# Kernel optimization log

Hardware: AMD Instinct MI355X
Metric: run time of the kernel (lower is better)

The kernel has to match this reference:

```python
import jax, jax.numpy as jnp
import numpy as np

ROT_DIM = 32  # rotary sub-dimension hardcoded in the original module


def apply_rope(x, rope):
    # x: [B, T, H, hd], rope: [T, ROT_DIM//2, 2]
    T = x.shape[1]
    rc = rope[:T][:, None]            # [T, 1, 16, 2]
    cos, sin = rc[..., 0], rc[..., 1]  # [T, 1, 16]
    x_rot, x_pass = x[..., :ROT_DIM], x[..., ROT_DIM:]
    x1, x2 = x_rot[..., :ROT_DIM // 2], x_rot[..., ROT_DIM // 2:]
    return jnp.concatenate([x1 * cos - x2 * sin, x2 * cos + x1 * sin, x_pass], axis=-1)


def setup_inputs() -> dict:
    key = jax.random.key(0)
    ks = jax.random.split(key, 6)
    B, T, C, H = 4, 1024, 2048, 32
    hd = C // H
    x = jax.random.normal(ks[0], (B, T, C), dtype=jnp.float32)
    mask = jnp.tril(jnp.ones((T, T), dtype=bool))  # causal, True = attend
    index = jnp.arange(T, dtype=jnp.int64) if jax.config.jax_enable_x64 else jnp.arange(T, dtype=jnp.int32)
    # realistic rotary cos/sin cache
    inv_freq = 1.0 / (10000.0 ** (np.arange(0, ROT_DIM, 2, dtype=np.float32) / ROT_DIM))
    ang = np.arange(T, dtype=np.float32)[:, None] * inv_freq[None, :]  # [T, 16]
    rope = jnp.asarray(np.stack([np.cos(ang), np.sin(ang)], axis=-1))   # [T, 16, 2]
    s = 1.0 / np.sqrt(C)
    Wqkv_w = jax.random.normal(ks[1], (3 * C, C), dtype=jnp.float32) * s
    Wqkv_b = jax.random.normal(ks[2], (3 * C,), dtype=jnp.float32) * 0.01
    out_w = jax.random.normal(ks[3], (C, C), dtype=jnp.float32) * s
    out_b = jax.random.normal(ks[4], (C,), dtype=jnp.float32) * 0.01
    k_cache = jnp.zeros((B, H, T, hd), dtype=jnp.float32)
    v_cache = jnp.zeros((B, H, T, hd), dtype=jnp.float32)
    return {"x": x, "mask": mask, "index": index, "rope": rope,
            "Wqkv_w": Wqkv_w, "Wqkv_b": Wqkv_b, "out_w": out_w, "out_b": out_b,
            "k_cache": k_cache, "v_cache": v_cache}


def reference(x, mask, index, rope, Wqkv_w, Wqkv_b, out_w, out_b, k_cache, v_cache):
    B, T, C = x.shape
    H = 32
    hd = C // H
    qkv = x @ Wqkv_w.T + Wqkv_b                 # [B, T, 3C]
    q, k, v = jnp.split(qkv, 3, axis=-1)
    q = q.reshape(B, T, H, hd)
    k = k.reshape(B, T, H, hd)
    v = v.reshape(B, T, H, hd)
    q = apply_rope(q, rope)
    k = apply_rope(k, rope)
    q = q.transpose(0, 2, 1, 3)                 # [B, H, T, hd]
    k = k.transpose(0, 2, 1, 3)
    v = v.transpose(0, 2, 1, 3)
    # KV-cache scatter update; index = arange(T) covers the full cache, so the
    # subsequent slice [:, :, :index[-1]+1] is the whole cache (static shape).
    k_full = k_cache.at[:, :, index].set(k)
    v_full = v_cache.at[:, :, index].set(v)
    scores = jnp.einsum('bhqd,bhkd->bhqk', q, k_full) / jnp.sqrt(jnp.asarray(hd, x.dtype))
    scores = jnp.where(mask, scores, jnp.finfo(x.dtype).min)
    attn = jax.nn.softmax(scores, axis=-1)
    ctx = jnp.einsum('bhqk,bhkd->bhqd', attn, v_full)
    ctx = ctx.transpose(0, 2, 1, 3).reshape(B, T, C)
    return ctx @ out_w.T + out_b
```

## Files before the change

kernel.cpp:

```cpp
#include <hip/hip_runtime.h>

typedef unsigned short u16;
typedef unsigned int u32;
typedef __bf16 bf16x8 __attribute__((ext_vector_type(8)));
typedef float floatx4 __attribute__((ext_vector_type(4)));
typedef u16 u16x4 __attribute__((ext_vector_type(4)));
typedef u16 u16x8 __attribute__((ext_vector_type(8)));
typedef u32 u32x2 __attribute__((ext_vector_type(2)));

#define B_ 4
#define T_ 1024
#define C_ 2048
#define H_ 32
#define HD_ 64

__device__ __forceinline__ float b2f(u16 u) {
    u32 x = ((u32)u) << 16;
    return __builtin_bit_cast(float, x);
}
__device__ __forceinline__ u16 f2b(float f) {
    u32 i = __builtin_bit_cast(u32, f);
    u32 r = (i + 0x7FFFu + ((i >> 16) & 1u)) >> 16;
    return (u16)r;
}
__device__ __forceinline__ u32 pack2(float a, float b) {
    const u32 ua = __builtin_bit_cast(u32, a) + 0x8000u;
    const u32 ub = __builtin_bit_cast(u32, b) + 0x8000u;
    return __builtin_amdgcn_perm(ub, ua, 0x07060302u);
}

#define GLOAD16(gp, lp) __builtin_amdgcn_global_load_lds( \
    (const __attribute__((address_space(1))) void*)(gp),  \
    (__attribute__((address_space(3))) void*)(lp), 16, 0, 0)

#define LGKM0() asm volatile("s_waitcnt lgkmcnt(0)" ::: "memory")

__global__ __launch_bounds__(256) void convert_all(const float* __restrict__ x,
                                                   const float* __restrict__ wqkv,
                                                   const float* __restrict__ outw,
                                                   u16* __restrict__ dst) {
    const int stride = gridDim.x * 256;
    for (int i = blockIdx.x * 256 + threadIdx.x; i < 6291456; i += stride) {
        const float* s;
        int off;
        if (i < 2097152) { s = x; off = i; }
        else if (i < 5242880) { s = wqkv; off = i - 2097152; }
        else { s = outw; off = i - 5242880; }
        const floatx4 v = *(const floatx4*)(s + (size_t)off * 4);
        const u32x2 h = {pack2(v.x, v.y), pack2(v.z, v.w)};
        *(u32x2*)(dst + (size_t)i * 4) = h;
    }
}

template <int MODE>
__global__ __launch_bounds__(256) void gemm_bt(const u16* __restrict__ A,
                                               const u16* __restrict__ W,
                                               const float* __restrict__ bias,
                                               const float* __restrict__ rope,
                                               void* __restrict__ o0v,
                                               u16* __restrict__ o1,
                                               u16* __restrict__ o2) {
    const int Kdim = 2048;
    __shared__ __align__(16) u16 As[128 * 64];
    __shared__ __align__(16) u16 Bs[128 * 64];

    const int tid = threadIdx.x;
    const int w = tid >> 6, lane = tid & 63;
    const int wr = w >> 1, wc = w & 1;
    const int quad = lane >> 4, l15 = lane & 15;
    const int mBase = blockIdx.y * 128, nBase = blockIdx.x * 128;

    floatx4 acc[4][4] = {};

    const int lrow = lane >> 3;
    const int lcol = ((lane & 7) ^ lrow) * 8;
    const u16* Ap = A + (size_t)(mBase + lrow) * Kdim + lcol;
    const u16* Wp = W + (size_t)(nBase + lrow) * Kdim + lcol;

    const int xk = l15 & 7;

    for (int k0 = 0; k0 < Kdim; k0 += 64) {
#pragma unroll
        for (int i = 0; i < 4; i++) {
            const int c = i * 4 + w;
            GLOAD16(Ap + (size_t)c * 8 * Kdim + k0, &As[c * 512]);
            GLOAD16(Wp + (size_t)c * 8 * Kdim + k0, &Bs[c * 512]);
        }
        __syncthreads();
#pragma unroll
        for (int ks = 0; ks < 64; ks += 32) {
            bf16x8 af[4], bfr[4];
#pragma unroll
            for (int i = 0; i < 4; i++) {
                const int co = (((ks >> 3) + quad) ^ xk) * 8;
                af[i] = *(const bf16x8*)&As[(wr * 64 + i * 16 + l15) * 64 + co];
            }
#pragma unroll
            for (int j = 0; j < 4; j++) {
                const int co = (((ks >> 3) + quad) ^ xk) * 8;
                bfr[j] = *(const bf16x8*)&Bs[(wc * 64 + j * 16 + l15) * 64 + co];
            }
#pragma unroll
            for (int i = 0; i < 4; i++)
#pragma unroll
                for (int j = 0; j < 4; j++)
                    acc[i][j] = __builtin_amdgcn_mfma_f32_16x16x32_bf16(af[i], bfr[j], acc[i][j], 0, 0, 0);
        }
        __syncthreads();
    }

    const int nq = nBase + wc * 64;
    float bv[4];
#pragma unroll
    for (int j = 0; j < 4; j++) bv[j] = bias[nq + j * 16 + l15];

    if (MODE == 0) {
        const int region = nq >> 11;
        const int h = (nq & 2047) >> 6;
        const int d = l15;
        u16* dst = (region == 0) ? (u16*)o0v : ((region == 1) ? o1 : o2);
#pragma unroll
        for (int i = 0; i < 4; i++) {
#pragma unroll
            for (int r = 0; r < 4; r++) {
                const int m = mBase + wr * 64 + i * 16 + quad * 4 + r;
                const int b = m >> 10, t = m & 1023;
                float v0 = acc[i][0][r] + bv[0];
                float v1 = acc[i][1][r] + bv[1];
                float v2 = acc[i][2][r] + bv[2];
                float v3 = acc[i][3][r] + bv[3];
                const size_t base = ((size_t)(b * H_ + h) * T_ + t) * HD_;
                if (region < 2) {
                    const float cz = rope[t * 32 + d * 2];
                    const float sz = rope[t * 32 + d * 2 + 1];
                    const float n0 = v0 * cz - v1 * sz;
                    const float n1 = v1 * cz + v0 * sz;
                    dst[base + d] = f2b(n0);
                    dst[base + 16 + d] = f2b(n1);
                } else {
                    dst[base + d] = f2b(v0);
                    dst[base + 16 + d] = f2b(v1);
                }
                dst[base + 32 + d] = f2b(v2);
                dst[base + 48 + d] = f2b(v3);
            }
        }
    } else {
        float* outf = (float*)o0v;
#pragma unroll
        for (int i = 0; i < 4; i++)
#pragma unroll
            for (int r = 0; r < 4; r++) {
                const int m = mBase + wr * 64 + i * 16 + quad * 4 + r;
                const size_t o = (size_t)m * 2048 + nq;
#pragma unroll
                for (int j = 0; j < 4; j++)
                    outf[o + j * 16 + l15] = acc[i][j][r] + bv[j];
            }
    }
}

#define VT_STR 72

#define LOADK(DST, KT)                                                         \
  {                                                                            \
    const u16* kp_ = kbase + (size_t)(KT) * 64 * HD_;                          \
    _Pragma("unroll") for (int mi = 0; mi < 4; mi++) {                         \
      const u16* kr_ = kp_ + (mi * 16 + l15) * HD_ + quad * 8;                 \
      DST[2 * mi]     = __builtin_bit_cast(bf16x8, *(const u16x8*)(kr_));      \
      DST[2 * mi + 1] = __builtin_bit_cast(bf16x8, *(const u16x8*)(kr_ + 32)); \
    }                                                                          \
  }

__global__ __launch_bounds__(256) void attn_mfma(const u16* __restrict__ qT,
                                                 const u16* __restrict__ kT,
                                                 const u16* __restrict__ vT,
                                                 u16* __restrict__ ctx) {
    __shared__ __align__(16) u16 Vt[2][64 * VT_STR];
    __shared__ __align__(16) u16 Pt[4 * 16 * VT_STR];

    const int tid = threadIdx.x;
    const int w = tid >> 6, lane = tid & 63;
    const int quad = lane >> 4, l15 = lane & 15;

    const int lin = (int)blockIdx.y * 8 + (int)blockIdx.x;
    const int xcd = lin & 7;
    const int jj = lin >> 3;
    const int pair = jj >> 4;
    const int bh = (jj & 15) * 8 + xcd;

    const size_t headBase = (size_t)bh * (T_ * HD_);

    u16* myPt = &Pt[w * 16 * VT_STR];
    const int vhd = tid & 63, vkb = tid >> 6;
    const float SC = 0.18033688011112042f;
    const u16* kbase = kT + headBase;

    int gb = 0;
#pragma unroll 1
    for (int ti = 0; ti < 2; ti++) {
        const int qt = ti ? (15 - pair) : pair;
        const int qrow = w * 16 + l15;

        bf16x8 qf[2];
        {
            const u16* qr = qT + headBase + ((size_t)qt * 64 + qrow) * HD_ + quad * 8;
            qf[0] = __builtin_bit_cast(bf16x8, *(const u16x8*)(qr));
            qf[1] = __builtin_bit_cast(bf16x8, *(const u16x8*)(qr + 32));
        }

        float m_i = -1e30f, l_i = 0.f;
        floatx4 oacc[4] = {};

        bf16x8 kC[8];
        LOADK(kC, 0)

#pragma unroll 1
        for (int kt = 0; kt <= qt; kt++) {
            const u16* vp = vT + headBase + (size_t)kt * 64 * HD_;

            u16 vreg[16];
#pragma unroll
            for (int c = 0; c < 16; c++)
                vreg[c] = vp[(vkb * 16 + c) * HD_ + vhd];

            floatx4 st[4] = {};
#pragma unroll
            for (int mi = 0; mi < 4; mi++) {
                st[mi] = __builtin_amdgcn_mfma_f32_16x16x32_bf16(kC[2 * mi], qf[0], st[mi], 0, 0, 0);
                st[mi] = __builtin_amdgcn_mfma_f32_16x16x32_bf16(kC[2 * mi + 1], qf[1], st[mi], 0, 0, 0);
            }

            if (kt < qt) LOADK(kC, kt + 1)

            u16* vt = Vt[gb];
#pragma unroll
            for (int c4 = 0; c4 < 4; c4++) {
                const u16x4 vv = {vreg[c4 * 4], vreg[c4 * 4 + 1], vreg[c4 * 4 + 2], vreg[c4 * 4 + 3]};
                *(u16x4*)&vt[vhd * VT_STR + vkb * 16 + c4 * 4] = vv;
            }
            LGKM0();
            __builtin_amdgcn_s_barrier();

            float pmax = -1e30f;
#pragma unroll
            for (int mi = 0; mi < 4; mi++)
#pragma unroll
                for (int r = 0; r < 4; r++) {
                    float sv = st[mi][r] * SC;
                    if (kt == qt && (mi * 16 + quad * 4 + r) > qrow) sv = -1e30f;
                    st[mi][r] = sv;
                    pmax = fmaxf(pmax, sv);
                }
            pmax = fmaxf(pmax, __shfl_xor(pmax, 16, 64));
            pmax = fmaxf(pmax, __shfl_xor(pmax, 32, 64));

            if (!__all(pmax <= m_i + 11.0f)) {
                const float mnew = fmaxf(m_i, pmax);
                const float alpha = __builtin_amdgcn_exp2f(m_i - mnew);
                m_i = mnew;
                l_i *= alpha;
#pragma unroll
                for (int mi = 0; mi < 4; mi++) oacc[mi] *= alpha;
            }

            float psum = 0.f;
#pragma unroll
            for (int mi = 0; mi < 4; mi++) {
                float p[4];
#pragma unroll
                for (int r = 0; r < 4; r++) {
                    p[r] = __builtin_amdgcn_exp2f(st[mi][r] - m_i);
                    psum += p[r];
                }
                const u32x2 pk2 = {pack2(p[0], p[1]), pack2(p[2], p[3])};
                *(u32x2*)&myPt[l15 * VT_STR + mi * 16 + quad * 4] = pk2;
            }
            psum += __shfl_xor(psum, 16, 64);
            psum += __shfl_xor(psum, 32, 64);
            l_i += psum;

            bf16x8 pf[2];
            pf[0] = __builtin_bit_cast(bf16x8, *(const u16x8*)&myPt[l15 * VT_STR + quad * 8]);
            pf[1] = __builtin_bit_cast(bf16x8, *(const u16x8*)&myPt[l15 * VT_STR + 32 + quad * 8]);
#pragma unroll
            for (int mi = 0; mi < 4; mi++) {
                const bf16x8 vf0 = __builtin_bit_cast(bf16x8, *(const u16x8*)&vt[(mi * 16 + l15) * VT_STR + quad * 8]);
                const bf16x8 vf1 = __builtin_bit_cast(bf16x8, *(const u16x8*)&vt[(mi * 16 + l15) * VT_STR + 32 + quad * 8]);
                oacc[mi] = __builtin_amdgcn_mfma_f32_16x16x32_bf16(vf0, pf[0], oacc[mi], 0, 0, 0);
                oacc[mi] = __builtin_amdgcn_mfma_f32_16x16x32_bf16(vf1, pf[1], oacc[mi], 0, 0, 0);
            }
            gb ^= 1;
        }

        const float inv = 1.0f / l_i;
        const int b = bh >> 5, h = bh & 31;
        const int t = qt * 64 + qrow;
        u16* cp = ctx + ((size_t)(b * T_ + t)) * C_ + h * HD_;
#pragma unroll
        for (int mi = 0; mi < 4; mi++) {
            const u16x4 ov = {f2b(oacc[mi][0] * inv), f2b(oacc[mi][1] * inv),
                              f2b(oacc[mi][2] * inv), f2b(oacc[mi][3] * inv)};
            *(u16x4*)(cp + mi * 16 + quad * 4) = ov;
        }
    }
}

extern "C" void kernel_launch(void* const* d_in, const int* in_sizes, int n_in,
                              void* d_out, int out_size, void* d_ws, size_t ws_size,
                              hipStream_t stream) {
    const float* x      = (const float*)d_in[0];
    const float* rope   = (const float*)d_in[3];
    const float* Wqkv_w = (const float*)d_in[4];
    const float* Wqkv_b = (const float*)d_in[5];
    const float* out_w  = (const float*)d_in[6];
    const float* out_b  = (const float*)d_in[7];
    float* out = (float*)d_out;

    const size_t headElems = (size_t)B_ * H_ * T_ * HD_;
    u16* xb    = (u16*)d_ws;
    u16* wqkvb = xb + headElems;
    u16* outwb = wqkvb + 12582912;
    u16* qTp   = outwb + 4194304;
    u16* kTp   = qTp + headElems;
    u16* vTp   = kTp + headElems;
    u16* ctx   = xb;

    convert_all<<<dim3(3072), 256, 0, stream>>>(x, Wqkv_w, out_w, xb);

    gemm_bt<0><<<dim3(48, 32), 256, 0, stream>>>(xb, wqkvb, Wqkv_b, rope, qTp, kTp, vTp);
    attn_mfma<<<dim3(8, 128), 256, 0, stream>>>(qTp, kTp, vTp, ctx);
    gemm_bt<1><<<dim3(16, 32), 256, 0, stream>>>(ctx, outwb, out_b, rope, out, nullptr, nullptr);
}
```

Baseline: 413.1 us.

## Process both causal query tiles in a single shared K/V loop

```diff
diff --git a/kernel.cpp b/kernel.cpp
--- a/kernel.cpp
+++ b/kernel.cpp
@@ -172,6 +172,72 @@
     }                                                                          \
   }
 
+#define QKC(ST, QF)                                                            \
+  _Pragma("unroll") for (int mi = 0; mi < 4; mi++) {                           \
+    ST[mi] = floatx4{};                                                        \
+    ST[mi] = __builtin_amdgcn_mfma_f32_16x16x32_bf16(kC[2 * mi], QF[0], ST[mi], 0, 0, 0);     \
+    ST[mi] = __builtin_amdgcn_mfma_f32_16x16x32_bf16(kC[2 * mi + 1], QF[1], ST[mi], 0, 0, 0); \
+  }
+
+#define SMAXW(ST, M_I, L_I, OACC, QT)                                          \
+  {                                                                            \
+    float pmax_ = -1e30f;                                                      \
+    const int diag_ = (kt == (QT));                                            \
+    _Pragma("unroll") for (int mi = 0; mi < 4; mi++)                           \
+      _Pragma("unroll") for (int r = 0; r < 4; r++) {                          \
+        float sv = ST[mi][r] * SC;                                             \
+        if (diag_ && (mi * 16 + quad * 4 + r) > qrow) sv = -1e30f;             \
+        ST[mi][r] = sv;                                                        \
+        pmax_ = fmaxf(pmax_, sv);                                              \
+      }                                                                        \
+    pmax_ = fmaxf(pmax_, __shfl_xor(pmax_, 16, 64));                           \
+    pmax_ = fmaxf(pmax_, __shfl_xor(pmax_, 32, 64));                           \
+    if (!__all(pmax_ <= M_I + 11.0f)) {                                        \
+      const float mnew_ = fmaxf(M_I, pmax_);                                   \
+      const float alpha_ = __builtin_amdgcn_exp2f(M_I - mnew_);                \
+      M_I = mnew_;                                                             \
+      L_I *= alpha_;                                                           \
+      _Pragma("unroll") for (int mi = 0; mi < 4; mi++) OACC[mi] *= alpha_;     \
+    }                                                                          \
+    float psum_ = 0.f;                                                         \
+    _Pragma("unroll") for (int mi = 0; mi < 4; mi++) {                         \
+      float p0 = __builtin_amdgcn_exp2f(ST[mi][0] - M_I);                      \
+      float p1 = __builtin_amdgcn_exp2f(ST[mi][1] - M_I);                      \
+      float p2 = __builtin_amdgcn_exp2f(ST[mi][2] - M_I);                      \
+      float p3 = __builtin_amdgcn_exp2f(ST[mi][3] - M_I);                      \
+      psum_ += p0 + p1 + p2 + p3;                                              \
+      const u32x2 pk2_ = {pack2(p0, p1), pack2(p2, p3)};                       \
+      *(u32x2*)&myPt[l15 * VT_STR + mi * 16 + quad * 4] = pk2_;                \
+    }                                                                          \
+    psum_ += __shfl_xor(psum_, 16, 64);                                        \
+    psum_ += __shfl_xor(psum_, 32, 64);                                        \
+    L_I += psum_;                                                              \
+  }
+
+#define PVACC(OACC, VTP)                                                       \
+  {                                                                            \
+    const bf16x8 pf0_ = __builtin_bit_cast(bf16x8, *(const u16x8*)&myPt[l15 * VT_STR + quad * 8]);      \
+    const bf16x8 pf1_ = __builtin_bit_cast(bf16x8, *(const u16x8*)&myPt[l15 * VT_STR + 32 + quad * 8]); \
+    _Pragma("unroll") for (int mi = 0; mi < 4; mi++) {                         \
+      const bf16x8 vf0_ = __builtin_bit_cast(bf16x8, *(const u16x8*)&(VTP)[(mi * 16 + l15) * VT_STR + quad * 8]);      \
+      const bf16x8 vf1_ = __builtin_bit_cast(bf16x8, *(const u16x8*)&(VTP)[(mi * 16 + l15) * VT_STR + 32 + quad * 8]); \
+      OACC[mi] = __builtin_amdgcn_mfma_f32_16x16x32_bf16(vf0_, pf0_, OACC[mi], 0, 0, 0);                \
+      OACC[mi] = __builtin_amdgcn_mfma_f32_16x16x32_bf16(vf1_, pf1_, OACC[mi], 0, 0, 0);                \
+    }                                                                          \
+  }
+
+#define STOREO(OACC, L_I, QT)                                                  \
+  {                                                                            \
+    const float inv_ = 1.0f / (L_I);                                           \
+    const int t_ = (QT) * 64 + qrow;                                           \
+    u16* cp_ = ctx + ((size_t)(bb * T_ + t_)) * C_ + hh * HD_;                 \
+    _Pragma("unroll") for (int mi = 0; mi < 4; mi++) {                         \
+      const u16x4 ov_ = {f2b(OACC[mi][0] * inv_), f2b(OACC[mi][1] * inv_),     \
+                         f2b(OACC[mi][2] * inv_), f2b(OACC[mi][3] * inv_)};    \
+      *(u16x4*)(cp_ + mi * 16 + quad * 4) = ov_;                               \
+    }                                                                          \
+  }
+
 __global__ __launch_bounds__(256) void attn_mfma(const u16* __restrict__ qT,
                                                  const u16* __restrict__ kT,
                                                  const u16* __restrict__ vT,
@@ -190,120 +256,71 @@
     const int bh = (jj & 15) * 8 + xcd;
 
     const size_t headBase = (size_t)bh * (T_ * HD_);
+    const int bb = bh >> 5, hh = bh & 31;
 
     u16* myPt = &Pt[w * 16 * VT_STR];
     const int vhd = tid & 63, vkb = tid >> 6;
     const float SC = 0.18033688011112042f;
     const u16* kbase = kT + headBase;
+    const int qrow = w * 16 + l15;
+
+    const int qtA = pair;
+    const int qtB = 15 - pair;
+
+    bf16x8 qfA[2], qfB[2];
+    {
+        const u16* qrA = qT + headBase + ((size_t)qtA * 64 + qrow) * HD_ + quad * 8;
+        qfA[0] = __builtin_bit_cast(bf16x8, *(const u16x8*)(qrA));
+        qfA[1] = __builtin_bit_cast(bf16x8, *(const u16x8*)(qrA + 32));
+        const u16* qrB = qT + headBase + ((size_t)qtB * 64 + qrow) * HD_ + quad * 8;
+        qfB[0] = __builtin_bit_cast(bf16x8, *(const u16x8*)(qrB));
+        qfB[1] = __builtin_bit_cast(bf16x8, *(const u16x8*)(qrB + 32));
+    }
+
+    float mA = -1e30f, lA = 0.f, mB = -1e30f, lB = 0.f;
+    floatx4 oaccA[4] = {}, oaccB[4] = {};
+
+    bf16x8 kC[8];
+    LOADK(kC, 0)
 
     int gb = 0;
 #pragma unroll 1
-    for (int ti = 0; ti < 2; ti++) {
-        const int qt = ti ? (15 - pair) : pair;
-        const int qrow = w * 16 + l15;
-
-        bf16x8 qf[2];
-        {
-            const u16* qr = qT + headBase + ((size_t)qt * 64 + qrow) * HD_ + quad * 8;
-            qf[0] = __builtin_bit_cast(bf16x8, *(const u16x8*)(qr));
-            qf[1] = __builtin_bit_cast(bf16x8, *(const u16x8*)(qr + 32));
-        }
-
-        float m_i = -1e30f, l_i = 0.f;
-        floatx4 oacc[4] = {};
-
-        bf16x8 kC[8];
-        LOADK(kC, 0)
-
-#pragma unroll 1
-        for (int kt = 0; kt <= qt; kt++) {
-            const u16* vp = vT + headBase + (size_t)kt * 64 * HD_;
-
-            u16 vreg[16];
-#pragma unroll
-            for (int c = 0; c < 16; c++)
-                vreg[c] = vp[(vkb * 16 + c) * HD_ + vhd];
-
-            floatx4 st[4] = {};
-#pragma unroll
-            for (int mi = 0; mi < 4; mi++) {
-                st[mi] = __builtin_amdgcn_mfma_f32_16x16x32_bf16(kC[2 * mi], qf[0], st[mi], 0, 0, 0);
-                st[mi] = __builtin_amdgcn_mfma_f32_16x16x32_bf16(kC[2 * mi + 1], qf[1], st[mi], 0, 0, 0);
-            }
-
-            if (kt < qt) LOADK(kC, kt + 1)
-
-            u16* vt = Vt[gb];
-#pragma unroll
-            for (int c4 = 0; c4 < 4; c4++) {
-                const u16x4 vv = {vreg[c4 * 4], vreg[c4 * 4 + 1], vreg[c4 * 4 + 2], vreg[c4 * 4 + 3]};
-                *(u16x4*)&vt[vhd * VT_STR + vkb * 16 + c4 * 4] = vv;
-            }
-            LGKM0();
-            __builtin_amdgcn_s_barrier();
-
-            float pmax = -1e30f;
-#pragma unroll
-            for (int mi = 0; mi < 4; mi++)
-#pragma unroll
-                for (int r = 0; r < 4; r++) {
-                    float sv = st[mi][r] * SC;
-                    if (kt == qt && (mi * 16 + quad * 4 + r) > qrow) sv = -1e30f;
-                    st[mi][r] = sv;
-                    pmax = fmaxf(pmax, sv);
-                }
-            pmax = fmaxf(pmax, __shfl_xor(pmax, 16, 64));
-            pmax = fmaxf(pmax, __shfl_xor(pmax, 32, 64));
-
-            if (!__all(pmax <= m_i + 11.0f)) {
-                const float mnew = fmaxf(m_i, pmax);
-                const float alpha = __builtin_amdgcn_exp2f(m_i - mnew);
-                m_i = mnew;
-                l_i *= alpha;
-#pragma unroll
-                for (int mi = 0; mi < 4; mi++) oacc[mi] *= alpha;
-            }
-
-            float psum = 0.f;
-#pragma unroll
-            for (int mi = 0; mi < 4; mi++) {
-                float p[4];
-#pragma unroll
-                for (int r = 0; r < 4; r++) {
-                    p[r] = __builtin_amdgcn_exp2f(st[mi][r] - m_i);
-                    psum += p[r];
-                }
-                const u32x2 pk2 = {pack2(p[0], p[1]), pack2(p[2], p[3])};
-                *(u32x2*)&myPt[l15 * VT_STR + mi * 16 + quad * 4] = pk2;
-            }
-            psum += __shfl_xor(psum, 16, 64);
-            psum += __shfl_xor(psum, 32, 64);
-            l_i += psum;
-
-            bf16x8 pf[2];
-            pf[0] = __builtin_bit_cast(bf16x8, *(const u16x8*)&myPt[l15 * VT_STR + quad * 8]);
-            pf[1] = __builtin_bit_cast(bf16x8, *(const u16x8*)&myPt[l15 * VT_STR + 32 + quad * 8]);
-#pragma unroll
-            for (int mi = 0; mi < 4; mi++) {
-                const bf16x8 vf0 = __builtin_bit_cast(bf16x8, *(const u16x8*)&vt[(mi * 16 + l15) * VT_STR + quad * 8]);
-                const bf16x8 vf1 = __builtin_bit_cast(bf16x8, *(const u16x8*)&vt[(mi * 16 + l15) * VT_STR + 32 + quad * 8]);
-                oacc[mi] = __builtin_amdgcn_mfma_f32_16x16x32_bf16(vf0, pf[0], oacc[mi], 0, 0, 0);
-                oacc[mi] = __builtin_amdgcn_mfma_f32_16x16x32_bf16(vf1, pf[1], oacc[mi], 0, 0, 0);
-            }
-            gb ^= 1;
-        }
-
-        const float inv = 1.0f / l_i;
-        const int b = bh >> 5, h = bh & 31;
-        const int t = qt * 64 + qrow;
-        u16* cp = ctx + ((size_t)(b * T_ + t)) * C_ + h * HD_;
-#pragma unroll
-        for (int mi = 0; mi < 4; mi++) {
-            const u16x4 ov = {f2b(oacc[mi][0] * inv), f2b(oacc[mi][1] * inv),
-                              f2b(oacc[mi][2] * inv), f2b(oacc[mi][3] * inv)};
-            *(u16x4*)(cp + mi * 16 + quad * 4) = ov;
-        }
-    }
+    for (int kt = 0; kt <= qtB; kt++) {
+        const int doA = (kt <= qtA);
+        const u16* vp = vT + headBase + (size_t)kt * 64 * HD_;
+
+        u16 vreg[16];
+#pragma unroll
+        for (int c = 0; c < 16; c++)
+            vreg[c] = vp[(vkb * 16 + c) * HD_ + vhd];
+
+        floatx4 st[4];
+        if (doA) {
+            QKC(st, qfA)
+            SMAXW(st, mA, lA, oaccA, qtA)
+        }
+        QKC(st, qfB)
+
+        if (kt < qtB) LOADK(kC, kt + 1)
+
+        u16* vt = Vt[gb];
+#pragma unroll
+        for (int c4 = 0; c4 < 4; c4++) {
+            const u16x4 vv = {vreg[c4 * 4], vreg[c4 * 4 + 1], vreg[c4 * 4 + 2], vreg[c4 * 4 + 3]};
+            *(u16x4*)&vt[vhd * VT_STR + vkb * 16 + c4 * 4] = vv;
+        }
+        LGKM0();
+        __builtin_amdgcn_s_barrier();
+
+        if (doA) { PVACC(oaccA, vt) }
+
+        SMAXW(st, mB, lB, oaccB, qtB)
+        PVACC(oaccB, vt)
+        gb ^= 1;
+    }
+
+    STOREO(oaccA, lA, qtA)
+    STOREO(oaccB, lB, qtB)
 }
 
 extern "C" void kernel_launch(void* const* d_in, const int* in_sizes, int n_in,
```

After: 407.0 us. About the same (-1.5%).
